# Kernel tuning notes

Measured on AMD Instinct MI355X. Metric: run time of the kernel, lower is better.

## Reference

```python
import jax, jax.numpy as jnp
import numpy as np
import math

N_LEVELS = 4          # quadtree depth; leaves = 4**4 = 256
N_HEAD = 8
LN_EPS = 1e-5

def _tree_consts():
    # level d has 4**d nodes; offsets[d] = first node index of level d
    sizes = [4 ** d for d in range(N_LEVELS + 1)]
    offsets = np.concatenate([[0], np.cumsum(sizes)])
    n_nodes = int(offsets[-1])  # 341
    parent = np.full(n_nodes, -1, np.int64)
    for d in range(1, N_LEVELS + 1):
        idx = offsets[d] + np.arange(sizes[d])
        parent[idx] = offsets[d - 1] + np.arange(sizes[d]) // 4
    # chain[c, k] = k-th ancestor of c (k=0 -> self); padded by clamping at root
    chain = np.zeros((n_nodes, N_LEVELS + 1), np.int64)
    chain[:, 0] = np.arange(n_nodes)
    for k in range(1, N_LEVELS + 1):
        prev = chain[:, k - 1]
        chain[:, k] = np.where(parent[prev] >= 0, parent[prev], prev)
    nodes_at = [offsets[d] + np.arange(sizes[d]) for d in range(N_LEVELS + 1)]
    return chain, nodes_at, n_nodes

CHAIN, NODES_AT, N_NODES = _tree_consts()

def layernorm(x, g, b):
    m = jnp.mean(x, -1, keepdims=True)
    v = jnp.var(x, -1, keepdims=True)
    return (x - m) * jax.lax.rsqrt(v + LN_EPS) * g + b

def mhsa(x, w_qkv, b_qkv, w_proj, b_proj):
    B, N, E = x.shape
    hd = E // N_HEAD
    qkv = x @ w_qkv + b_qkv                       # (B, N, 3E)
    q, k, v = jnp.split(qkv, 3, axis=-1)
    sh = lambda t: t.reshape(B, N, N_HEAD, hd).transpose(0, 2, 1, 3)  # (B,H,N,hd)
    q, k, v = sh(q), sh(k), sh(v)
    att = jax.nn.softmax(jnp.einsum('bhqd,bhkd->bhqk', q, k) / math.sqrt(hd), axis=-1)
    o = jnp.einsum('bhqk,bhkd->bhqd', att, v).transpose(0, 2, 1, 3).reshape(B, N, E)
    return o @ w_proj + b_proj

def branch_mlp(x, M, b1, w2, b2):
    # Sparse equivalent of einsum('bni,bjmni->bmj', x, W1): W1[:, c, a, :]
    # is nonzero only for a in {c} U ancestors(c), with the weight matrix
    # depending only on (depth(c), depth(a)). Group nodes by depth and sum
    # over ancestor offsets k (depth(a) = d - k).
    B, N, E = x.shape
    h = jnp.zeros((B, N, 4 * E), x.dtype)
    for d in range(N_LEVELS + 1):
        nd = NODES_AT[d]                           # static numpy indices
        acc = jnp.zeros((B, nd.shape[0], 4 * E), x.dtype)
        for k in range(d + 1):
            src = CHAIN[nd, k]                     # ancestor at depth d-k
            acc = acc + jnp.einsum('bne,je->bnj', x[:, src, :], M[d, d - k])
        h = h.at[:, nd, :].set(acc)
    h = jax.nn.relu(h + b1[None, :, :])
    return h @ w2 + b2

def setup_inputs() -> dict:
    key = jax.random.key(0)
    ks = jax.random.split(key, 6)
    B, N, E = 64, N_NODES, 512
    s = 0.02
    return {
        'x': jax.random.normal(ks[0], (B, N, E), jnp.float32),
        'ln1_g': jnp.ones((E,), jnp.float32),
        'ln1_b': jnp.zeros((E,), jnp.float32),
        'w_qkv': jax.random.normal(ks[1], (E, 3 * E), jnp.float32) * s,
        'b_qkv': jnp.zeros((3 * E,), jnp.float32),
        'w_proj': jax.random.normal(ks[2], (E, E), jnp.float32) * s,
        'b_proj': jnp.zeros((E,), jnp.float32),
        'ln2_g': jnp.ones((E,), jnp.float32),
        'ln2_b': jnp.zeros((E,), jnp.float32),
        'mlp_M': jax.random.normal(ks[3], (N_LEVELS + 1, N_LEVELS + 1, 4 * E, E), jnp.float32) * s,
        'mlp_b1': jnp.zeros((N, 4 * E), jnp.float32),
        'w2': jax.random.normal(ks[4], (4 * E, E), jnp.float32) * s,
        'b2': jnp.zeros((E,), jnp.float32),
    }

def reference(x, ln1_g, ln1_b, w_qkv, b_qkv, w_proj, b_proj,
              ln2_g, ln2_b, mlp_M, mlp_b1, w2, b2):
    x = x + mhsa(layernorm(x, ln1_g, ln1_b), w_qkv, b_qkv, w_proj, b_proj)
    x = x + branch_mlp(layernorm(x, ln2_g, ln2_b), mlp_M, mlp_b1, w2, b2)
    return x
```

## Files before the change

### kernel.cpp

```cpp
#include <hip/hip_runtime.h>
#include <hip/hip_bf16.h>


typedef __attribute__((ext_vector_type(8))) __bf16 bf16x8;
typedef __attribute__((ext_vector_type(4))) float f32x4;
typedef __attribute__((ext_vector_type(4))) unsigned int u32x4;

#define GF_RELU    1
#define GF_OUTBF16 2

static __device__ __forceinline__ bf16x8 bzero8() {
    u32x4 z = {0u, 0u, 0u, 0u};
    return __builtin_bit_cast(bf16x8, z);
}

__global__ void transpose_bf16_kernel(const float* __restrict__ in,
                                      __hip_bfloat16* __restrict__ out,
                                      int K, int N, int log2K) {
    int idx = blockIdx.x * 256 + threadIdx.x;
    if (idx >= K * N) return;
    int n = idx >> log2K;
    int k = idx & (K - 1);
    out[idx] = __float2bfloat16(in[(size_t)k * N + n]);
}

__global__ void pack_wcat_kernel(const float* __restrict__ M,
                                 __hip_bfloat16* __restrict__ out) {
    int p = blockIdx.y;
    int s, d;
    if (p < 5)       { s = 0; d = p; }
    else if (p < 9)  { s = 1; d = p - 4; }
    else if (p < 12) { s = 2; d = p - 7; }
    else if (p < 14) { s = 3; d = p - 9; }
    else             { s = 4; d = 4; }
    const int base_lut[5] = {0, 5, 9, 12, 14};
    size_t idx = (size_t)blockIdx.x * 256 + threadIdx.x;
    const size_t MB = 2048ull * 512;
    out[(size_t)base_lut[s] * MB + (size_t)(d - s) * MB + idx] =
        __float2bfloat16(M[((size_t)d * 5 + s) * MB + idx]);
}

__global__ __launch_bounds__(256) void ln_kernel(const float* __restrict__ x,
                                                 const float* __restrict__ g,
                                                 const float* __restrict__ b,
                                                 __hip_bfloat16* __restrict__ out) {
    int tok = blockIdx.x;
    const float* xr = x + (size_t)tok * 512;
    int t = threadIdx.x;
    float v0 = xr[t], v1 = xr[t + 256];
    float s = v0 + v1;
    float s2 = v0 * v0 + v1 * v1;
    #pragma unroll
    for (int o = 32; o > 0; o >>= 1) {
        s  += __shfl_down(s, o);
        s2 += __shfl_down(s2, o);
    }
    __shared__ float ps[4], ps2[4];
    int w = t >> 6, lane = t & 63;
    if (lane == 0) { ps[w] = s; ps2[w] = s2; }
    __syncthreads();
    if (t == 0) {
        float ts = 0.f, ts2 = 0.f;
        #pragma unroll
        for (int i = 0; i < 4; i++) { ts += ps[i]; ts2 += ps2[i]; }
        ps[0] = ts * (1.f / 512.f);
        ps2[0] = ts2 * (1.f / 512.f);
    }
    __syncthreads();
    float m = ps[0];
    float var = ps2[0] - m * m;
    float r = rsqrtf(var + 1e-5f);
    out[(size_t)tok * 512 + t]       = __float2bfloat16((v0 - m) * r * g[t] + b[t]);
    out[(size_t)tok * 512 + t + 256] = __float2bfloat16((v1 - m) * r * g[t + 256] + b[t + 256]);
}

#define ATT_STR 72
__global__ __launch_bounds__(256) void attn_mfma_kernel(const __hip_bfloat16* __restrict__ qkv,
                                                        __hip_bfloat16* __restrict__ ctx) {
    __shared__ __bf16 kt_lds[64 * ATT_STR];
    __shared__ __bf16 vt_lds[64 * ATT_STR];
    __shared__ __bf16 pbuf[4 * 48 * ATT_STR];

    const int bh = blockIdx.x;
    const int half = blockIdx.y;
    const int b = bh >> 3, h = bh & 7;
    const int tid = threadIdx.x;
    const int w = tid >> 6, lane = tid & 63;
    const int q = lane >> 4, l16 = lane & 15;
    const int rowbase = half * 192 + w * 48;
    __bf16* pw = pbuf + w * 48 * ATT_STR;

    bf16x8 qf[3][2];
    #pragma unroll
    for (int mi = 0; mi < 3; mi++) {
        int row = rowbase + mi * 16 + l16;
        #pragma unroll
        for (int ks = 0; ks < 2; ks++) {
            if (row < 341)
                qf[mi][ks] = *(const bf16x8*)(qkv + (size_t)(b * 341 + row) * 1536 +
                                              h * 64 + ks * 32 + q * 8);
            else
                qf[mi][ks] = bzero8();
        }
    }

    f32x4 O[3][4];
    float mrun[3][4], lrun[3][4];
    #pragma unroll
    for (int mi = 0; mi < 3; mi++) {
        #pragma unroll
        for (int ni = 0; ni < 4; ni++) { f32x4 z = {0.f,0.f,0.f,0.f}; O[mi][ni] = z; }
        #pragma unroll
        for (int rr = 0; rr < 4; rr++) { mrun[mi][rr] = -1e30f; lrun[mi][rr] = 0.f; }
    }

    for (int kt6 = 0; kt6 < 6; kt6++) {
        const int kbase = kt6 * 64;
        __syncthreads();
        {
            int key = tid >> 2, kg = tid & 3;
            int gk = kbase + key;
            bf16x8 a0 = bzero8(), a1 = bzero8();
            if (gk < 341) {
                const __hip_bfloat16* src =
                    qkv + (size_t)(b * 341 + gk) * 1536 + 512 + h * 64 + kg * 16;
                a0 = *(const bf16x8*)src;
                a1 = *(const bf16x8*)(src + 8);
            }
            *(bf16x8*)(kt_lds + key * ATT_STR + kg * 16)     = a0;
            *(bf16x8*)(kt_lds + key * ATT_STR + kg * 16 + 8) = a1;
        }
        {
            int key = tid & 63, dg = tid >> 6;
            int gk = kbase + key;
            bf16x8 a0 = bzero8(), a1 = bzero8();
            if (gk < 341) {
                const __hip_bfloat16* src =
                    qkv + (size_t)(b * 341 + gk) * 1536 + 1024 + h * 64 + dg * 16;
                a0 = *(const bf16x8*)src;
                a1 = *(const bf16x8*)(src + 8);
            }
            #pragma unroll
            for (int j = 0; j < 8; j++) {
                vt_lds[(dg * 16 + j) * ATT_STR + key]     = a0[j];
                vt_lds[(dg * 16 + 8 + j) * ATT_STR + key] = a1[j];
            }
        }
        __syncthreads();

        f32x4 S[3][4];
        #pragma unroll
        for (int mi = 0; mi < 3; mi++)
            #pragma unroll
            for (int ni = 0; ni < 4; ni++) { f32x4 z = {0.f,0.f,0.f,0.f}; S[mi][ni] = z; }
        #pragma unroll
        for (int ks = 0; ks < 2; ks++) {
            bf16x8 bf_[4];
            #pragma unroll
            for (int ni = 0; ni < 4; ni++)
                bf_[ni] = *(const bf16x8*)(kt_lds + (ni * 16 + l16) * ATT_STR + ks * 32 + q * 8);
            #pragma unroll
            for (int mi = 0; mi < 3; mi++)
                #pragma unroll
                for (int ni = 0; ni < 4; ni++)
                    S[mi][ni] = __builtin_amdgcn_mfma_f32_16x16x32_bf16(qf[mi][ks], bf_[ni],
                                                                        S[mi][ni], 0, 0, 0);
        }

        float cmask[4];
        #pragma unroll
        for (int ni = 0; ni < 4; ni++)
            cmask[ni] = (kbase + ni * 16 + l16 < 341) ? 0.f : -1e30f;

        #pragma unroll
        for (int mi = 0; mi < 3; mi++) {
            #pragma unroll
            for (int rr = 0; rr < 4; rr++) {
                float rmax = -1e30f;
                #pragma unroll
                for (int ni = 0; ni < 4; ni++)
                    rmax = fmaxf(rmax, fmaf(S[mi][ni][rr], 0.125f, cmask[ni]));
                rmax = fmaxf(rmax, __shfl_xor(rmax, 1));
                rmax = fmaxf(rmax, __shfl_xor(rmax, 2));
                rmax = fmaxf(rmax, __shfl_xor(rmax, 4));
                rmax = fmaxf(rmax, __shfl_xor(rmax, 8));
                float mnew = fmaxf(mrun[mi][rr], rmax);
                float alpha = __expf(mrun[mi][rr] - mnew);
                mrun[mi][rr] = mnew;
                float psum = 0.f;
                #pragma unroll
                for (int ni = 0; ni < 4; ni++) {
                    float p = __expf(fmaf(S[mi][ni][rr], 0.125f, cmask[ni]) - mnew);
                    S[mi][ni][rr] = p;
                    psum += p;
                    O[mi][ni][rr] *= alpha;
                }
                psum += __shfl_xor(psum, 1);
                psum += __shfl_xor(psum, 2);
                psum += __shfl_xor(psum, 4);
                psum += __shfl_xor(psum, 8);
                lrun[mi][rr] = lrun[mi][rr] * alpha + psum;
            }
            #pragma unroll
            for (int ni = 0; ni < 4; ni++)
                #pragma unroll
                for (int rr = 0; rr < 4; rr++)
                    pw[(mi * 16 + q * 4 + rr) * ATT_STR + ni * 16 + l16] =
                        (__bf16)S[mi][ni][rr];
        }
        __syncthreads();

        #pragma unroll
        for (int ks = 0; ks < 2; ks++) {
            bf16x8 pf[3], vf[4];
            #pragma unroll
            for (int mi = 0; mi < 3; mi++)
                pf[mi] = *(const bf16x8*)(pw + (mi * 16 + l16) * ATT_STR + ks * 32 + q * 8);
            #pragma unroll
            for (int ni = 0; ni < 4; ni++)
                vf[ni] = *(const bf16x8*)(vt_lds + (ni * 16 + l16) * ATT_STR + ks * 32 + q * 8);
            #pragma unroll
            for (int mi = 0; mi < 3; mi++)
                #pragma unroll
                for (int ni = 0; ni < 4; ni++)
                    O[mi][ni] = __builtin_amdgcn_mfma_f32_16x16x32_bf16(pf[mi], vf[ni],
                                                                        O[mi][ni], 0, 0, 0);
        }
    }

    #pragma unroll
    for (int mi = 0; mi < 3; mi++) {
        #pragma unroll
        for (int rr = 0; rr < 4; rr++) {
            int row = rowbase + mi * 16 + q * 4 + rr;
            if (row >= 341) continue;
            float inv = 1.f / lrun[mi][rr];
            __hip_bfloat16* op = ctx + (size_t)(b * 341 + row) * 512 + h * 64;
            #pragma unroll
            for (int ni = 0; ni < 4; ni++)
                op[ni * 16 + l16] = __float2bfloat16(O[mi][ni][rr] * inv);
        }
    }
}

template <bool GATHER>
static __device__ __forceinline__ void gemm128_body(
    __hip_bfloat16* As, __hip_bfloat16* Bs,
    const __hip_bfloat16* __restrict__ A, const __hip_bfloat16* __restrict__ Bt,
    const float* __restrict__ bias, const float* __restrict__ resid,
    float* __restrict__ Cf, __hip_bfloat16* __restrict__ Cb,
    int Mrows, int N, int K, int flags, int depth, int bm0, int bn0) {
    const int tid = threadIdx.x;
    const int r = tid >> 1;
    const int kh = (tid & 1) << 4;
    const int gr = bm0 + r;
    const int gn = bn0 + r;
    const int lane = tid & 63;
    const int w = tid >> 6;
    const int wm = (w >> 1) << 6;
    const int wn = (w & 1) << 6;
    const int q = lane >> 4;
    const int l16 = lane & 15;

    size_t abase;
    if (GATHER) {
        const int dsh = depth << 1;
        const int bmask = (1 << dsh) - 1;
        int b = gr >> dsh;
        int i = gr & bmask;
        int node = (0x55555555 & bmask) + i;
        abase = ((size_t)(b * 341 + node)) << 9;
    } else {
        abase = (size_t)gr * K;
    }

    f32x4 acc[4][4];
    #pragma unroll
    for (int i = 0; i < 4; i++)
        #pragma unroll
        for (int j = 0; j < 4; j++) {
            f32x4 z = {0.f, 0.f, 0.f, 0.f};
            acc[i][j] = z;
        }

    for (int k0 = 0; k0 < K; k0 += 32) {
        bf16x8 va0 = bzero8(), va1 = bzero8(), vb0, vb1;
        if (gr < Mrows) {
            const bf16x8* p = (const bf16x8*)(A + abase + k0 + kh);
            va0 = p[0];
            va1 = p[1];
        }
        {
            const bf16x8* p = (const bf16x8*)(Bt + (size_t)gn * K + k0 + kh);
            vb0 = p[0];
            vb1 = p[1];
        }
        __syncthreads();
        *(bf16x8*)(As + r * 32 + kh)     = va0;
        *(bf16x8*)(As + r * 32 + kh + 8) = va1;
        *(bf16x8*)(Bs + r * 32 + kh)     = vb0;
        *(bf16x8*)(Bs + r * 32 + kh + 8) = vb1;
        __syncthreads();
        bf16x8 af[4], bfr[4];
        #pragma unroll
        for (int mi = 0; mi < 4; mi++)
            af[mi] = *(const bf16x8*)(As + (wm + mi * 16 + l16) * 32 + q * 8);
        #pragma unroll
        for (int ni = 0; ni < 4; ni++)
            bfr[ni] = *(const bf16x8*)(Bs + (wn + ni * 16 + l16) * 32 + q * 8);
        #pragma unroll
        for (int mi = 0; mi < 4; mi++)
            #pragma unroll
            for (int ni = 0; ni < 4; ni++)
                acc[mi][ni] = __builtin_amdgcn_mfma_f32_16x16x32_bf16(
                    af[mi], bfr[ni], acc[mi][ni], 0, 0, 0);
    }

    #pragma unroll
    for (int mi = 0; mi < 4; mi++) {
        #pragma unroll
        for (int rr = 0; rr < 4; rr++) {
            int grow = bm0 + wm + mi * 16 + q * 4 + rr;
            if (grow >= Mrows) continue;
            size_t obase = (size_t)grow * N;
            #pragma unroll
            for (int ni = 0; ni < 4; ni++) {
                int col = bn0 + wn + ni * 16 + l16;
                float v = acc[mi][ni][rr];
                if (bias) v += bias[col];
                if (resid) v += resid[obase + col];
                if (flags & GF_RELU) v = fmaxf(v, 0.f);
                if (flags & GF_OUTBF16)
                    Cb[obase + col] = __float2bfloat16(v);
                else
                    Cf[obase + col] = v;
            }
        }
    }
}

static __device__ __forceinline__ int xcd_remap(int bid, int nwg) {
    const int xcd = bid & 7, o = bid >> 3;
    const int qq = nwg >> 3, rr = nwg & 7;
    return (xcd < rr ? xcd * (qq + 1) : rr * (qq + 1) + (xcd - rr) * qq) + o;
}

__global__ __launch_bounds__(256) void gemm128(
    const __hip_bfloat16* __restrict__ A, const __hip_bfloat16* __restrict__ Bt,
    const float* __restrict__ bias, const float* __restrict__ resid,
    float* __restrict__ Cf, __hip_bfloat16* __restrict__ Cb,
    int Mrows, int N, int K, int flags, int gridN) {
    __shared__ __hip_bfloat16 As[128 * 32];
    __shared__ __hip_bfloat16 Bs[128 * 32];
    const int lin = xcd_remap(blockIdx.x, gridDim.x);
    const int bx = lin / gridN;
    const int by = lin - bx * gridN;
    gemm128_body<false>(As, Bs, A, Bt, bias, resid, Cf, Cb,
                        Mrows, N, K, flags, 0, bx << 7, by << 7);
}

__global__ __launch_bounds__(256) void gemm_branch_fused(
    const __hip_bfloat16* __restrict__ xn, const __hip_bfloat16* __restrict__ wcat,
    __hip_bfloat16* __restrict__ Y) {
    __shared__ __hip_bfloat16 As[128 * 32];
    __shared__ __hip_bfloat16 Bs[128 * 32];
    const int lin = xcd_remap(blockIdx.x, gridDim.x);
    int s;
    if (lin < 80)        s = 0;
    else if (lin < 208)  s = 1;
    else if (lin < 592)  s = 2;
    else if (lin < 1616) s = 3;
    else                 s = 4;
    const int base_tab[5] = {0, 80, 208, 592, 1616};
    const int gn_tab[5]   = {80, 64, 48, 32, 16};
    const size_t yoff[5]  = {0, 655360, 2752512, 9043968, 25821184};
    const int wcat_off[5] = {0, 5, 9, 12, 14};
    const int loc = lin - base_tab[s];
    const int gn = gn_tab[s];
    const int bx = loc / gn;
    const int by = loc - bx * gn;
    const int Mrows = 64 << (s << 1);
    const int N = (5 - s) << 11;
    gemm128_body<true>(As, Bs, xn, wcat + (size_t)wcat_off[s] * (2048ull * 512),
                       nullptr, nullptr, nullptr, Y + yoff[s],
                       Mrows, N, 512, GF_OUTBF16, s, bx << 7, by << 7);
}

__global__ __launch_bounds__(256) void combine_kernel(const __hip_bfloat16* __restrict__ Y,
                                                      const float* __restrict__ b1,
                                                      __hip_bfloat16* __restrict__ h) {
    const size_t yoff[5] = {0, 655360, 2752512, 9043968, 25821184};
    int row = blockIdx.x;
    int b = row / 341;
    int node = row - b * 341;
    int d = (node >= 85) ? 4 : (node >= 21) ? 3 : (node >= 5) ? 2 : (node >= 1) ? 1 : 0;
    int i = node - (0x55555555 & ((1 << (d << 1)) - 1));
    int j = threadIdx.x << 3;

    float acc[8];
    const float* bp = b1 + (size_t)node * 2048 + j;
    f32x4 b0 = *(const f32x4*)bp;
    f32x4 b4 = *(const f32x4*)(bp + 4);
    #pragma unroll
    for (int u = 0; u < 4; u++) { acc[u] = b0[u]; acc[u + 4] = b4[u]; }

    #pragma unroll
    for (int s = 0; s < 5; s++) {
        if (s <= d) {
            int a = i >> ((d - s) << 1);
            int width = (5 - s) << 11;
            const bf16x8 v = *(const bf16x8*)(Y + yoff[s] +
                (size_t)((b << (s << 1)) + a) * width + ((d - s) << 11) + j);
            #pragma unroll
            for (int u = 0; u < 8; u++) acc[u] += (float)v[u];
        }
    }
    bf16x8 o;
    #pragma unroll
    for (int u = 0; u < 8; u++) o[u] = (__bf16)fmaxf(acc[u], 0.f);
    *(bf16x8*)(h + (size_t)row * 2048 + j) = o;
}

extern "C" void kernel_launch(void* const* d_in, const int* in_sizes, int n_in,
                              void* d_out, int out_size, void* d_ws, size_t ws_size,
                              hipStream_t stream) {
    const float* x      = (const float*)d_in[0];
    const float* ln1_g  = (const float*)d_in[1];
    const float* ln1_b  = (const float*)d_in[2];
    const float* w_qkv  = (const float*)d_in[3];
    const float* b_qkv  = (const float*)d_in[4];
    const float* w_proj = (const float*)d_in[5];
    const float* b_proj = (const float*)d_in[6];
    const float* ln2_g  = (const float*)d_in[7];
    const float* ln2_b  = (const float*)d_in[8];
    const float* mlp_M  = (const float*)d_in[9];
    const float* mlp_b1 = (const float*)d_in[10];
    const float* w2     = (const float*)d_in[11];
    const float* b2     = (const float*)d_in[12];
    float* out = (float*)d_out;

    const int M = 64 * 341;

    char* ws = (char*)d_ws;
    size_t off = 0;
    auto alloc = [&](size_t bytes) -> char* {
        char* p = ws + off;
        off += (bytes + 255) & ~(size_t)255;
        return p;
    };
    __hip_bfloat16* xn     = (__hip_bfloat16*)alloc((size_t)M * 512 * 2);
    __hip_bfloat16* wqkvT  = (__hip_bfloat16*)alloc(1536ull * 512 * 2);
    __hip_bfloat16* wprojT = (__hip_bfloat16*)alloc(512ull * 512 * 2);
    __hip_bfloat16* w2T    = (__hip_bfloat16*)alloc(512ull * 2048 * 2);
    __hip_bfloat16* wcat   = (__hip_bfloat16*)alloc(15ull * 2048 * 512 * 2);
    __hip_bfloat16* hbuf   = (__hip_bfloat16*)alloc((size_t)M * 2048 * 2);
    const size_t qkv_bytes = (size_t)M * 1536 * 2;
    const size_t y_bytes   = 59375616ull * 2;
    char* shared = alloc(y_bytes);
    __hip_bfloat16* qkv = (__hip_bfloat16*)shared;
    __hip_bfloat16* ctx = (__hip_bfloat16*)(shared + qkv_bytes);
    __hip_bfloat16* Y   = (__hip_bfloat16*)shared;
    if (off > ws_size) return;

    auto g128 = [&](const __hip_bfloat16* A, const __hip_bfloat16* Bt,
                    const float* bias, const float* resid, float* Cf,
                    __hip_bfloat16* Cb, int Mr, int N, int K, int flags) {
        int gm = (Mr + 127) >> 7, gn = N >> 7;
        gemm128<<<dim3(gm * gn), 256, 0, stream>>>(
            A, Bt, bias, resid, Cf, Cb, Mr, N, K, flags, gn);
    };

    transpose_bf16_kernel<<<(512 * 1536 + 255) / 256, 256, 0, stream>>>(w_qkv, wqkvT, 512, 1536, 9);
    transpose_bf16_kernel<<<(512 * 512 + 255) / 256, 256, 0, stream>>>(w_proj, wprojT, 512, 512, 9);
    transpose_bf16_kernel<<<(2048 * 512 + 255) / 256, 256, 0, stream>>>(w2, w2T, 2048, 512, 11);
    pack_wcat_kernel<<<dim3(4096, 15), 256, 0, stream>>>(mlp_M, wcat);

    ln_kernel<<<M, 256, 0, stream>>>(x, ln1_g, ln1_b, xn);
    g128(xn, wqkvT, b_qkv, nullptr, nullptr, qkv, M, 1536, 512, GF_OUTBF16);
    attn_mfma_kernel<<<dim3(512, 2), 256, 0, stream>>>(qkv, ctx);
    g128(ctx, wprojT, b_proj, x, out, nullptr, M, 512, 512, 0);

    ln_kernel<<<M, 256, 0, stream>>>(out, ln2_g, ln2_b, xn);
    gemm_branch_fused<<<dim3(3664), 256, 0, stream>>>(xn, wcat, Y);
    combine_kernel<<<M, 256, 0, stream>>>(Y, mlp_b1, hbuf);
    g128(hbuf, w2T, b2, out, out, nullptr, M, 512, 2048, 0);
}
```

Before: 785.3 us.

## Double GEMM K-tile to 64 with XOR-swizzled shared memory layout

The shared GEMM body now stages 64-wide K slices instead of 32, so each barrier pair is followed by two MFMA k-steps. This halves the number of __syncthreads per K and issues wider global loads. The LDS tile is XOR-swizzled by row to avoid bank conflicts on the 128-byte row stride. The cost is twice the LDS per block and more registers for the staged vectors, which may reduce occupancy.

After: 751.5 us. -4.3%, faster.

```diff
diff --git a/kernel.cpp b/kernel.cpp
--- a/kernel.cpp
+++ b/kernel.cpp
@@ -252,7 +252,7 @@
     int Mrows, int N, int K, int flags, int depth, int bm0, int bn0) {
     const int tid = threadIdx.x;
     const int r = tid >> 1;
-    const int kh = (tid & 1) << 4;
+    const int khalf = tid & 1;
     const int gr = bm0 + r;
     const int gn = bn0 + r;
     const int lane = tid & 63;
@@ -261,6 +261,13 @@
     const int wn = (w & 1) << 6;
     const int q = lane >> 4;
     const int l16 = lane & 15;
+
+    int wsl[4];
+    #pragma unroll
+    for (int j = 0; j < 4; j++)
+        wsl[j] = ((((khalf << 2) | j) ^ (r & 7)) << 3);
+    const int rs0 = ((q ^ (l16 & 7)) << 3);
+    const int rs1 = (((4 + q) ^ (l16 & 7)) << 3);
 
     size_t abase;
     if (GATHER) {
@@ -283,37 +290,49 @@
             acc[i][j] = z;
         }
 
-    for (int k0 = 0; k0 < K; k0 += 32) {
-        bf16x8 va0 = bzero8(), va1 = bzero8(), vb0, vb1;
+    for (int k0 = 0; k0 < K; k0 += 64) {
+        bf16x8 va[4], vb[4];
         if (gr < Mrows) {
-            const bf16x8* p = (const bf16x8*)(A + abase + k0 + kh);
-            va0 = p[0];
-            va1 = p[1];
+            const bf16x8* p = (const bf16x8*)(A + abase + k0 + (khalf << 5));
+            #pragma unroll
+            for (int j = 0; j < 4; j++) va[j] = p[j];
+        } else {
+            #pragma unroll
+            for (int j = 0; j < 4; j++) va[j] = bzero8();
         }
         {
-            const bf16x8* p = (const bf16x8*)(Bt + (size_t)gn * K + k0 + kh);
-            vb0 = p[0];
-            vb1 = p[1];
+            const bf16x8* p = (const bf16x8*)(Bt + (size_t)gn * K + k0 + (khalf << 5));
+            #pragma unroll
+            for (int j = 0; j < 4; j++) vb[j] = p[j];
         }
         __syncthreads();
-        *(bf16x8*)(As + r * 32 + kh)     = va0;
-        *(bf16x8*)(As + r * 32 + kh + 8) = va1;
-        *(bf16x8*)(Bs + r * 32 + kh)     = vb0;
-        *(bf16x8*)(Bs + r * 32 + kh + 8) = vb1;
+        #pragma unroll
+        for (int j = 0; j < 4; j++) {
+            *(bf16x8*)(As + r * 64 + wsl[j]) = va[j];
+            *(bf16x8*)(Bs + r * 64 + wsl[j]) = vb[j];
+        }
         __syncthreads();
-        bf16x8 af[4], bfr[4];
-        #pragma unroll
-        for (int mi = 0; mi < 4; mi++)
-            af[mi] = *(const bf16x8*)(As + (wm + mi * 16 + l16) * 32 + q * 8);
-        #pragma unroll
-        for (int ni = 0; ni < 4; ni++)
-            bfr[ni] = *(const bf16x8*)(Bs + (wn + ni * 16 + l16) * 32 + q * 8);
-        #pragma unroll
-        for (int mi = 0; mi < 4; mi++)
-            #pragma unroll
-            for (int ni = 0; ni < 4; ni++)
-                acc[mi][ni] = __builtin_amdgcn_mfma_f32_16x16x32_bf16(
-                    af[mi], bfr[ni], acc[mi][ni], 0, 0, 0);
+        bf16x8 af[4][2], bfr[4][2];
+        #pragma unroll
+        for (int mi = 0; mi < 4; mi++) {
+            const __hip_bfloat16* rp = As + (wm + mi * 16 + l16) * 64;
+            af[mi][0] = *(const bf16x8*)(rp + rs0);
+            af[mi][1] = *(const bf16x8*)(rp + rs1);
+        }
+        #pragma unroll
+        for (int ni = 0; ni < 4; ni++) {
+            const __hip_bfloat16* rp = Bs + (wn + ni * 16 + l16) * 64;
+            bfr[ni][0] = *(const bf16x8*)(rp + rs0);
+            bfr[ni][1] = *(const bf16x8*)(rp + rs1);
+        }
+        #pragma unroll
+        for (int ks = 0; ks < 2; ks++)
+            #pragma unroll
+            for (int mi = 0; mi < 4; mi++)
+                #pragma unroll
+                for (int ni = 0; ni < 4; ni++)
+                    acc[mi][ni] = __builtin_amdgcn_mfma_f32_16x16x32_bf16(
+                        af[mi][ks], bfr[ni][ks], acc[mi][ni], 0, 0, 0);
     }
 
     #pragma unroll
@@ -350,8 +369,8 @@
     const float* __restrict__ bias, const float* __restrict__ resid,
     float* __restrict__ Cf, __hip_bfloat16* __restrict__ Cb,
     int Mrows, int N, int K, int flags, int gridN) {
-    __shared__ __hip_bfloat16 As[128 * 32];
-    __shared__ __hip_bfloat16 Bs[128 * 32];
+    __shared__ __hip_bfloat16 As[128 * 64];
+    __shared__ __hip_bfloat16 Bs[128 * 64];
     const int lin = xcd_remap(blockIdx.x, gridDim.x);
     const int bx = lin / gridN;
     const int by = lin - bx * gridN;
@@ -362,8 +381,8 @@
 __global__ __launch_bounds__(256) void gemm_branch_fused(
     const __hip_bfloat16* __restrict__ xn, const __hip_bfloat16* __restrict__ wcat,
     __hip_bfloat16* __restrict__ Y) {
-    __shared__ __hip_bfloat16 As[128 * 32];
-    __shared__ __hip_bfloat16 Bs[128 * 32];
+    __shared__ __hip_bfloat16 As[128 * 64];
+    __shared__ __hip_bfloat16 Bs[128 * 64];
     const int lin = xcd_remap(blockIdx.x, gridDim.x);
     int s;
     if (lin < 80)        s = 0;
```
